# Kernel tuning notes

Hardware: AMD Instinct MI355X
Metric: run time of the kernel (lower is better)

## Reference

```python
import jax, jax.numpy as jnp
import numpy as np

T, B, I, H = 512, 64, 512, 512

def _glorot(key, shape):
    fan_in, fan_out = shape
    std = np.sqrt(2.0 / (fan_in + fan_out))
    return (jax.random.normal(key, shape, dtype=jnp.float32) * std)

def setup_inputs() -> dict:
    key = jax.random.key(0)
    ks = jax.random.split(key, 9)
    inp = {"X": jax.random.normal(ks[0], (T, B, I), dtype=jnp.float32)}
    names = ["Wa_x", "Wi_x", "Wf_x", "Wo_x"]
    for n, k in zip(names, ks[1:5]):
        inp[n] = _glorot(k, (I, H))
    names_h = ["Wa_h", "Wi_h", "Wf_h", "Wo_h"]
    for n, k in zip(names_h, ks[5:9]):
        inp[n] = _glorot(k, (H, H))
    for n in ["ba", "bi", "bf", "bo"]:
        inp[n] = jnp.zeros((H,), dtype=jnp.float32)
    return inp

def reference(X, Wa_x, Wi_x, Wf_x, Wo_x, Wa_h, Wi_h, Wf_h, Wo_h, ba, bi, bf, bo):
    # Precompute input projections for all timesteps: [T,B,H] each
    Xa = jnp.einsum('tbi,ih->tbh', X, Wa_x) + ba
    Xi = jnp.einsum('tbi,ih->tbh', X, Wi_x) + bi
    Xf = jnp.einsum('tbi,ih->tbh', X, Wf_x) + bf
    Xo = jnp.einsum('tbi,ih->tbh', X, Wo_x) + bo

    def step(carry, xt):
        h, s = carry
        xa, xi, xf, xo = xt
        # At t=0 h=0 and s=0, which matches the original's special-cased first step
        a = jnp.tanh(xa + h @ Wa_h)
        i = jax.nn.sigmoid(xi + h @ Wi_h)
        f = jax.nn.sigmoid(xf + h @ Wf_h)
        o = jax.nn.sigmoid(xo + h @ Wo_h)
        s_new = a * i + s * f
        h_new = jnp.tanh(s_new) * o
        return (h_new, s_new), h_new

    h0 = jnp.zeros((B, H), dtype=X.dtype)
    s0 = jnp.zeros((B, H), dtype=X.dtype)
    _, hs = jax.lax.scan(step, (h0, s0), (Xa, Xi, Xf, Xo))
    return hs  # [T, B, H] (return_sequences=True)
```

## Files before the change

### kernel.cpp

```cpp
#include <hip/hip_runtime.h>
#include <cmath>


typedef __attribute__((ext_vector_type(8)))  short   short8;
typedef __attribute__((ext_vector_type(4)))  short   short4v;
typedef __attribute__((ext_vector_type(4)))  float   f32x4;
typedef __attribute__((ext_vector_type(16))) float   f32x16;

#define TSTEPS 512

__device__ __forceinline__ unsigned short f2bf(float f) {
  unsigned u = __builtin_bit_cast(unsigned, f);
  unsigned r = (u + 0x7FFFu + ((u >> 16) & 1u)) >> 16;
  return (unsigned short)r;
}
__device__ __forceinline__ float bf2f(unsigned short s) {
  unsigned u = ((unsigned)s) << 16;
  return __builtin_bit_cast(float, u);
}
__device__ __forceinline__ void gload_lds16(const void* g, void* l) {
  __builtin_amdgcn_global_load_lds(
      (const __attribute__((address_space(1))) unsigned int*)g,
      (__attribute__((address_space(3))) unsigned int*)l, 16, 0, 0);
}
__device__ __forceinline__ float sigmoid_fast(float x) {
  return 1.0f / (1.0f + __expf(-x));
}
__device__ __forceinline__ float tanh_fast(float x) {
  float e = __expf(2.0f * x);
  return 1.0f - 2.0f / (e + 1.0f);
}

__global__ __launch_bounds__(256) void prep_wT(
    const float* __restrict__ Wax, const float* __restrict__ Wix,
    const float* __restrict__ Wfx, const float* __restrict__ Wox,
    const float* __restrict__ Wah, const float* __restrict__ Wih,
    const float* __restrict__ Wfh, const float* __restrict__ Woh,
    unsigned short* __restrict__ WxT, unsigned short* __restrict__ WhT) {
  __shared__ float tile[32][33];
  int bx = blockIdx.x;
  int mat = bx >> 8;
  int t32 = bx & 255;
  int k0 = (t32 & 15) * 32;
  int h0 = (t32 >> 4) * 32;
  const float* S =
      (mat == 0) ? Wax : (mat == 1) ? Wix : (mat == 2) ? Wfx :
      (mat == 3) ? Wox : (mat == 4) ? Wah : (mat == 5) ? Wih :
      (mat == 6) ? Wfh : Woh;
  unsigned short* D = (mat < 4) ? WxT : WhT;
  int g = mat & 3;
  int tx = threadIdx.x & 31, ty = threadIdx.x >> 5;
#pragma unroll
  for (int r = 0; r < 4; ++r)
    tile[ty + r * 8][tx] = S[(size_t)(k0 + ty + r * 8) * 512 + h0 + tx];
  __syncthreads();
#pragma unroll
  for (int r = 0; r < 4; ++r) {
    int h = h0 + ty + r * 8;
    int k = k0 + tx;
    D[((size_t)(g * 512 + h) << 9) + k] = f2bf(tile[tx][ty + r * 8]);
  }
}

__global__ __launch_bounds__(256) void prep_xbf(const float* __restrict__ X,
                                                unsigned short* __restrict__ Xbf) {
  size_t i = (size_t)blockIdx.x * 256 + threadIdx.x;
  f32x4 v = *(const f32x4*)(X + i * 4);
  short4v o;
  o[0] = (short)f2bf(v[0]); o[1] = (short)f2bf(v[1]);
  o[2] = (short)f2bf(v[2]); o[3] = (short)f2bf(v[3]);
  *(short4v*)(Xbf + i * 4) = o;
}

__global__ __launch_bounds__(256) void prep_bias(
    const float* __restrict__ ba, const float* __restrict__ bi,
    const float* __restrict__ bf, const float* __restrict__ bo,
    float* __restrict__ biascat) {
  int n = blockIdx.x * 256 + threadIdx.x;
  int g = n >> 9, h = n & 511;
  const float* s = (g == 0) ? ba : (g == 1) ? bi : (g == 2) ? bf : bo;
  biascat[n] = s[h];
}

__global__ __launch_bounds__(256) void gemm_xproj(
    const unsigned short* __restrict__ Xbf,
    const unsigned short* __restrict__ WxT,
    const float* __restrict__ biascat,
    unsigned short* __restrict__ Xg) {
  __shared__ unsigned short Asm[128 * 64];
  __shared__ unsigned short Bsm[128 * 64];
  int bx = blockIdx.x;
  int nt = bx & 15, mt = bx >> 4;
  int m0 = mt * 128, n0 = nt * 128;
  int tid = threadIdx.x;
  int w = tid >> 6, l = tid & 63;
  int wm = (w >> 1) * 64, wn = (w & 1) * 64;
  f32x4 acc[4][4] = {};

  for (int ks = 0; ks < 8; ++ks) {
    int k0 = ks * 64;
    __syncthreads();
    int lr = l >> 3;
    int ksl = ((l & 7) ^ lr) * 8;
#pragma unroll
    for (int ii = 0; ii < 4; ++ii) {
      int i = w * 4 + ii;
      int r = i * 8 + lr;
      gload_lds16(Xbf + (size_t)(m0 + r) * 512 + k0 + ksl, Asm + i * 512 + l * 8);
    }
#pragma unroll
    for (int ii = 0; ii < 4; ++ii) {
      int i = w * 4 + ii;
      int r = i * 8 + lr;
      gload_lds16(WxT + (size_t)(n0 + r) * 512 + k0 + ksl, Bsm + i * 512 + l * 8);
    }
    __syncthreads();
#pragma unroll
    for (int kk = 0; kk < 2; ++kk) {
      short8 af[4], bfr[4];
#pragma unroll
      for (int mi = 0; mi < 4; ++mi) {
        int row = wm + mi * 16 + (l & 15);
        int slot = (kk * 4 + (l >> 4)) ^ (row & 7);
        af[mi] = *(const short8*)(Asm + row * 64 + slot * 8);
      }
#pragma unroll
      for (int ni = 0; ni < 4; ++ni) {
        int row = wn + ni * 16 + (l & 15);
        int slot = (kk * 4 + (l >> 4)) ^ (row & 7);
        bfr[ni] = *(const short8*)(Bsm + row * 64 + slot * 8);
      }
#pragma unroll
      for (int mi = 0; mi < 4; ++mi)
#pragma unroll
        for (int ni = 0; ni < 4; ++ni)
          acc[mi][ni] = __builtin_amdgcn_mfma_f32_16x16x32_bf16(
              af[mi], bfr[ni], acc[mi][ni], 0, 0, 0);
    }
  }
#pragma unroll
  for (int mi = 0; mi < 4; ++mi)
#pragma unroll
    for (int ni = 0; ni < 4; ++ni) {
      int col = n0 + wn + ni * 16 + (l & 15);
      float bias = biascat[col];
      int g = col >> 9, h = col & 511;
      int chunk = h >> 3, e = h & 7;
#pragma unroll
      for (int r = 0; r < 4; ++r) {
        int m = m0 + wm + mi * 16 + (l >> 4) * 4 + r;
        int t = m >> 6, b = m & 63;
        Xg[(((size_t)(t * 4 + g) * 64 + chunk) * 64 + b) * 8 + e] =
            f2bf(acc[mi][ni][r] + bias);
      }
    }
}

__global__ __launch_bounds__(256, 1) void lstm_scan(
    const unsigned short* __restrict__ Xg,
    const unsigned short* __restrict__ WhT,
    unsigned short* __restrict__ hbuf,
    int* __restrict__ flags,
    float* __restrict__ out) {
  const int j = blockIdx.x;
  const int mi = j & 1;
  const int cc = j >> 1;
  const int tid = threadIdx.x;
  const int w = tid >> 6, l = tid & 63;

  short8 wf[32];
  {
    const int m = l & 31;
    const int g = m >> 3;
    const int hcol_w = cc * 32 + w * 8 + (m & 7);
    const unsigned short* base =
        WhT + (((size_t)(g * 512 + hcol_w)) << 9) + (l >> 5) * 8;
#pragma unroll
    for (int kt = 0; kt < 32; ++kt) wf[kt] = *(const short8*)(base + kt * 16);
  }

  const int b = mi * 32 + (l & 31);
  const int hcol0 = cc * 32 + w * 8 + (l >> 5) * 4;
  const int mychunk = cc * 4 + w;

  const unsigned ld_voff0 = (unsigned)((l >> 5) * 1024 + b * 16);
  const unsigned st_voff = (unsigned)(mychunk * 1024 + b * 16 + (l >> 5) * 8);

  int* const myflag = flags + (mi * 16 + cc) * 32;
  int* const pollflag = flags + (mi * 16 + (l & 15)) * 32;

  float s4[4] = {0.f, 0.f, 0.f, 0.f};

  uint2 xgn[4];
#pragma unroll
  for (int g = 0; g < 4; ++g)
    xgn[g] = *(const uint2*)(Xg +
        ((((size_t)(0 * 4 + g) * 64 + mychunk) * 64 + b) * 8 + (l >> 5) * 4));

#pragma unroll 1
  for (int t = 0; t < TSTEPS; ++t) {
    f32x16 asum = {};
    if (t > 0) {
      int fv;
      do {
        fv = __hip_atomic_load(pollflag, __ATOMIC_RELAXED,
                               __HIP_MEMORY_SCOPE_AGENT);
      } while (!__all(fv >= t));
      asm volatile("" ::: "memory");
      const unsigned short* hbase = hbuf + (size_t)((t - 1) & 1) * 32768;
      short8 bfrag[32];
#pragma unroll
      for (int kt = 0; kt < 32; ++kt) {
        asm volatile("global_load_dwordx4 %0, %1, %2 sc0 sc1"
                     : "=v"(bfrag[kt])
                     : "v"(ld_voff0 + (unsigned)(kt * 2048)), "s"(hbase));
      }
      asm volatile("s_waitcnt vmcnt(0)" ::: "memory");
      __builtin_amdgcn_sched_barrier(0);
      f32x16 a0 = {}, a1 = {};
#pragma unroll
      for (int kt = 0; kt < 32; kt += 2) {
        a0 = __builtin_amdgcn_mfma_f32_32x32x16_bf16(wf[kt], bfrag[kt], a0,
                                                     0, 0, 0);
        a1 = __builtin_amdgcn_mfma_f32_32x32x16_bf16(wf[kt + 1], bfrag[kt + 1],
                                                     a1, 0, 0, 0);
      }
      asum = a0 + a1;
    }
    float hout[4];
#pragma unroll
    for (int q = 0; q < 4; ++q) {
      float pa = asum[0 * 4 + q] + bf2f((unsigned short)((q < 2 ? xgn[0].x : xgn[0].y) >> ((q & 1) * 16)));
      float pi = asum[1 * 4 + q] + bf2f((unsigned short)((q < 2 ? xgn[1].x : xgn[1].y) >> ((q & 1) * 16)));
      float pf = asum[2 * 4 + q] + bf2f((unsigned short)((q < 2 ? xgn[2].x : xgn[2].y) >> ((q & 1) * 16)));
      float po = asum[3 * 4 + q] + bf2f((unsigned short)((q < 2 ? xgn[3].x : xgn[3].y) >> ((q & 1) * 16)));
      float a  = tanh_fast(pa);
      float ig = sigmoid_fast(pi);
      float fg = sigmoid_fast(pf);
      float og = sigmoid_fast(po);
      s4[q] = a * ig + s4[q] * fg;
      hout[q] = tanh_fast(s4[q]) * og;
    }
    {
      unsigned lo = (unsigned)f2bf(hout[0]) | ((unsigned)f2bf(hout[1]) << 16);
      unsigned hi = (unsigned)f2bf(hout[2]) | ((unsigned)f2bf(hout[3]) << 16);
      uint2 hd; hd.x = lo; hd.y = hi;
      const unsigned short* sbase = hbuf + (size_t)(t & 1) * 32768;
      asm volatile("global_store_dwordx2 %0, %1, %2 sc0 sc1"
                   :: "v"(st_voff), "v"(hd), "s"(sbase) : "memory");
      asm volatile("s_waitcnt vmcnt(0)" ::: "memory");
      __syncthreads();
      if (tid == 0)
        __hip_atomic_store(myflag, t + 1, __ATOMIC_RELAXED,
                           __HIP_MEMORY_SCOPE_AGENT);
    }
    f32x4 ov;
    ov[0] = hout[0]; ov[1] = hout[1]; ov[2] = hout[2]; ov[3] = hout[3];
    *(f32x4*)(out + ((size_t)t * 64 + b) * 512 + hcol0) = ov;
    const int tn = (t + 1 < TSTEPS) ? t + 1 : t;
#pragma unroll
    for (int g = 0; g < 4; ++g)
      xgn[g] = *(const uint2*)(Xg +
          ((((size_t)(tn * 4 + g) * 64 + mychunk) * 64 + b) * 8 + (l >> 5) * 4));
  }
}

extern "C" void kernel_launch(void* const* d_in, const int* in_sizes, int n_in,
                              void* d_out, int out_size, void* d_ws,
                              size_t ws_size, hipStream_t stream) {
  const float* X   = (const float*)d_in[0];
  const float* Wax = (const float*)d_in[1];
  const float* Wix = (const float*)d_in[2];
  const float* Wfx = (const float*)d_in[3];
  const float* Wox = (const float*)d_in[4];
  const float* Wah = (const float*)d_in[5];
  const float* Wih = (const float*)d_in[6];
  const float* Wfh = (const float*)d_in[7];
  const float* Woh = (const float*)d_in[8];
  const float* ba  = (const float*)d_in[9];
  const float* bi  = (const float*)d_in[10];
  const float* bf  = (const float*)d_in[11];
  const float* bo  = (const float*)d_in[12];

  char* ws = (char*)d_ws;
  unsigned short* Xg   = (unsigned short*)(ws);
  unsigned short* Xbf  = (unsigned short*)(ws + 134217728);
  unsigned short* hbuf = (unsigned short*)(ws + 134217728);
  unsigned short* WxT  = (unsigned short*)(ws + 167772160);
  unsigned short* WhT  = (unsigned short*)(ws + 169869312);
  float*          bcat = (float*)(ws + 171966464);
  int*            flags= (int*)(ws + 171974656);

  hipMemsetAsync(ws + 171974656, 0, 4096, stream);

  prep_wT<<<2048, 256, 0, stream>>>(Wax, Wix, Wfx, Wox, Wah, Wih, Wfh, Woh,
                                    WxT, WhT);
  prep_xbf<<<16384, 256, 0, stream>>>(X, Xbf);
  prep_bias<<<8, 256, 0, stream>>>(ba, bi, bf, bo, bcat);
  gemm_xproj<<<4096, 256, 0, stream>>>(Xbf, WxT, bcat, Xg);
  lstm_scan<<<32, 256, 0, stream>>>(Xg, WhT, hbuf, flags, (float*)d_out);
}
```

Measured before the change: 1.982 ms.

## Tag hidden-state values with timestep to replace flag waits with data validation

Each bf16 hidden value is now stored in a 32-bit word whose high half holds the timestep tag. Consumers validate the tags on the loaded data and re-issue a sub-block's loads until it is fresh, pipelining four sub-blocks with the MFMAs. The producer no longer waits for its store to complete before the barrier, which shortens the per-step critical path. In exchange, hidden-state traffic doubles, some reloads may repeat, and the flag poll is kept, so there is now a second synchronization layer.

```diff
diff --git a/kernel.cpp b/kernel.cpp
--- a/kernel.cpp
+++ b/kernel.cpp
@@ -6,6 +6,7 @@
 typedef __attribute__((ext_vector_type(4)))  short   short4v;
 typedef __attribute__((ext_vector_type(4)))  float   f32x4;
 typedef __attribute__((ext_vector_type(16))) float   f32x16;
+typedef __attribute__((ext_vector_type(4)))  unsigned uint4v;
 
 #define TSTEPS 512
 
@@ -17,6 +18,9 @@
 __device__ __forceinline__ float bf2f(unsigned short s) {
   unsigned u = ((unsigned)s) << 16;
   return __builtin_bit_cast(float, u);
+}
+__device__ __forceinline__ unsigned umin_(unsigned a, unsigned b) {
+  return a < b ? a : b;
 }
 __device__ __forceinline__ void gload_lds16(const void* g, void* l) {
   __builtin_amdgcn_global_load_lds(
@@ -180,11 +184,12 @@
   }
 
   const int b = mi * 32 + (l & 31);
-  const int hcol0 = cc * 32 + w * 8 + (l >> 5) * 4;
+  const int half = l >> 5;
+  const int hcol0 = cc * 32 + w * 8 + half * 4;
   const int mychunk = cc * 4 + w;
 
-  const unsigned ld_voff0 = (unsigned)((l >> 5) * 1024 + b * 16);
-  const unsigned st_voff = (unsigned)(mychunk * 1024 + b * 16 + (l >> 5) * 8);
+  const unsigned st_voff = (unsigned)((cc * 8 + w * 2 + half) * 1024 + b * 16);
+  const unsigned ld_voff0 = (unsigned)(half * 2048 + b * 16);
 
   int* const myflag = flags + (mi * 16 + cc) * 32;
   int* const pollflag = flags + (mi * 16 + (l & 15)) * 32;
@@ -195,7 +200,18 @@
 #pragma unroll
   for (int g = 0; g < 4; ++g)
     xgn[g] = *(const uint2*)(Xg +
-        ((((size_t)(0 * 4 + g) * 64 + mychunk) * 64 + b) * 8 + (l >> 5) * 4));
+        ((((size_t)(0 * 4 + g) * 64 + mychunk) * 64 + b) * 8 + half * 4));
+
+#define ISSUE_SUB(sub_)                                                      \
+  {                                                                          \
+    _Pragma("unroll") for (int ii = 0; ii < 8; ++ii) {                       \
+      unsigned vo = ld_voff0 + (unsigned)(((sub_) * 8 + ii) * 4096);         \
+      asm volatile("global_load_dwordx4 %0, %1, %2 sc0 sc1"                  \
+                   : "=v"(u[2 * ii]) : "v"(vo), "s"(hbase));                 \
+      asm volatile("global_load_dwordx4 %0, %1, %2 sc0 sc1"                  \
+                   : "=v"(u[2 * ii + 1]) : "v"(vo + 1024u), "s"(hbase));     \
+    }                                                                        \
+  }
 
 #pragma unroll 1
   for (int t = 0; t < TSTEPS; ++t) {
@@ -207,23 +223,44 @@
                                __HIP_MEMORY_SCOPE_AGENT);
       } while (!__all(fv >= t));
       asm volatile("" ::: "memory");
-      const unsigned short* hbase = hbuf + (size_t)((t - 1) & 1) * 32768;
-      short8 bfrag[32];
-#pragma unroll
-      for (int kt = 0; kt < 32; ++kt) {
-        asm volatile("global_load_dwordx4 %0, %1, %2 sc0 sc1"
-                     : "=v"(bfrag[kt])
-                     : "v"(ld_voff0 + (unsigned)(kt * 2048)), "s"(hbase));
-      }
-      asm volatile("s_waitcnt vmcnt(0)" ::: "memory");
-      __builtin_amdgcn_sched_barrier(0);
+      const unsigned short* hbase = hbuf + (size_t)((t - 1) & 1) * 65536;
+      const unsigned wantHi = ((unsigned)t) << 16;
       f32x16 a0 = {}, a1 = {};
-#pragma unroll
-      for (int kt = 0; kt < 32; kt += 2) {
-        a0 = __builtin_amdgcn_mfma_f32_32x32x16_bf16(wf[kt], bfrag[kt], a0,
-                                                     0, 0, 0);
-        a1 = __builtin_amdgcn_mfma_f32_32x32x16_bf16(wf[kt + 1], bfrag[kt + 1],
-                                                     a1, 0, 0, 0);
+      uint4v u[16];
+      ISSUE_SUB(0);
+#pragma unroll
+      for (int sub = 0; sub < 4; ++sub) {
+        while (true) {
+          asm volatile("s_waitcnt vmcnt(0)" ::: "memory");
+          __builtin_amdgcn_sched_barrier(0);
+          unsigned mv = 0xFFFFFFFFu;
+#pragma unroll
+          for (int ii = 0; ii < 16; ++ii) {
+            uint4v q = u[ii];
+            mv = umin_(mv, umin_(umin_(q[0], q[1]), umin_(q[2], q[3])));
+          }
+          if (__all(mv >= wantHi)) break;
+          ISSUE_SUB(sub);
+        }
+        short8 pb[8];
+#pragma unroll
+        for (int ii = 0; ii < 8; ++ii) {
+          uint4v q0 = u[2 * ii], q1 = u[2 * ii + 1];
+          uint4v p;
+          p[0] = __builtin_amdgcn_perm(q0[1], q0[0], 0x05040100u);
+          p[1] = __builtin_amdgcn_perm(q0[3], q0[2], 0x05040100u);
+          p[2] = __builtin_amdgcn_perm(q1[1], q1[0], 0x05040100u);
+          p[3] = __builtin_amdgcn_perm(q1[3], q1[2], 0x05040100u);
+          pb[ii] = __builtin_bit_cast(short8, p);
+        }
+        if (sub < 3) ISSUE_SUB(sub + 1);
+#pragma unroll
+        for (int ii = 0; ii < 8; ii += 2) {
+          a0 = __builtin_amdgcn_mfma_f32_32x32x16_bf16(wf[sub * 8 + ii],
+                                                       pb[ii], a0, 0, 0, 0);
+          a1 = __builtin_amdgcn_mfma_f32_32x32x16_bf16(wf[sub * 8 + ii + 1],
+                                                       pb[ii + 1], a1, 0, 0, 0);
+        }
       }
       asum = a0 + a1;
     }
@@ -242,14 +279,16 @@
       hout[q] = tanh_fast(s4[q]) * og;
     }
     {
-      unsigned lo = (unsigned)f2bf(hout[0]) | ((unsigned)f2bf(hout[1]) << 16);
-      unsigned hi = (unsigned)f2bf(hout[2]) | ((unsigned)f2bf(hout[3]) << 16);
-      uint2 hd; hd.x = lo; hd.y = hi;
-      const unsigned short* sbase = hbuf + (size_t)(t & 1) * 32768;
-      asm volatile("global_store_dwordx2 %0, %1, %2 sc0 sc1"
+      const unsigned tg = ((unsigned)(t + 1)) << 16;
+      uint4v hd;
+      hd[0] = tg | (unsigned)f2bf(hout[0]);
+      hd[1] = tg | (unsigned)f2bf(hout[1]);
+      hd[2] = tg | (unsigned)f2bf(hout[2]);
+      hd[3] = tg | (unsigned)f2bf(hout[3]);
+      const unsigned short* sbase = hbuf + (size_t)(t & 1) * 65536;
+      asm volatile("global_store_dwordx4 %0, %1, %2 sc0 sc1"
                    :: "v"(st_voff), "v"(hd), "s"(sbase) : "memory");
-      asm volatile("s_waitcnt vmcnt(0)" ::: "memory");
-      __syncthreads();
+      __builtin_amdgcn_s_barrier();
       if (tid == 0)
         __hip_atomic_store(myflag, t + 1, __ATOMIC_RELAXED,
                            __HIP_MEMORY_SCOPE_AGENT);
@@ -261,8 +300,9 @@
 #pragma unroll
     for (int g = 0; g < 4; ++g)
       xgn[g] = *(const uint2*)(Xg +
-          ((((size_t)(tn * 4 + g) * 64 + mychunk) * 64 + b) * 8 + (l >> 5) * 4));
-  }
+          ((((size_t)(tn * 4 + g) * 64 + mychunk) * 64 + b) * 8 + half * 4));
+  }
+#undef ISSUE_SUB
 }
 
 extern "C" void kernel_launch(void* const* d_in, const int* in_sizes, int n_in,
@@ -298,5 +338,6 @@
   prep_xbf<<<16384, 256, 0, stream>>>(X, Xbf);
   prep_bias<<<8, 256, 0, stream>>>(ba, bi, bf, bo, bcat);
   gemm_xproj<<<4096, 256, 0, stream>>>(Xbf, WxT, bcat, Xg);
+  hipMemsetAsync(ws + 134217728, 0, 262144, stream);
   lstm_scan<<<32, 256, 0, stream>>>(Xg, WhT, hbuf, flags, (float*)d_out);
 }
```

After: 2.474 ms. 24.8% more time.
